# Kernel optimization log

Measured on AMD Instinct MI355X. Metric: run time of the kernel, lower is better.

Reference implementation:

```python
import jax, jax.numpy as jnp
import numpy as np

NPRE = 8        # diffusion iterations (production default 8000; math identical per step)
DEPS = 0.1
LAMBDA = 0.24
K_PM = 0.03     # exp(log(0.03)) buffer in the 'none' branch
ALPHA = 0.7
SIGMA_FREQ = 0.1


def _g_pm(x, K):
    # Perona-Malik conductance g(x) = 1 / (1 + |x^2| / K^2)
    return 1.0 / (1.0 + jnp.abs(x * x) / (K * K))


def _gaussian_blur3(x, sigma):
    # Replicates torch create_gaussian_kernel(3, sigma): linspace(-3//2, 3//2, 3) = [-2, -0.5, 1]
    xs = jnp.linspace(-2.0, 1.0, 3)
    g1 = jnp.exp(-(xs ** 2) / (2.0 * sigma * sigma))
    g1 = g1 / g1.sum()
    k2 = jnp.outer(g1, g1).astype(x.dtype)            # [3,3]
    C = x.shape[1]
    k = jnp.broadcast_to(k2, (C, 1, 3, 3))
    xp = jnp.pad(x, ((0, 0), (0, 0), (1, 1), (1, 1)), mode='reflect')
    return jax.lax.conv_general_dilated(
        xp, k, window_strides=(1, 1), padding='VALID',
        dimension_numbers=('NCHW', 'OIHW', 'NCHW'), feature_group_count=C)


def _edge_coeffs(I, K):
    # c(I): FFT high-pass edge response + finite differences -> Perona-Malik coefficients
    b, c_, h, w = I.shape
    F = jnp.fft.fft2(I, norm='ortho')
    y = jnp.linspace(-1.0, 1.0, h)[:, None]
    xg = jnp.linspace(-1.0, 1.0, w)[None, :]
    hf_mask = (jnp.sqrt(xg * xg + y * y) > 0.5).astype(I.dtype)   # [h,w]
    er = jnp.real(jnp.fft.ifft2(F * hf_mask, norm='ortho'))
    dv = jnp.abs(I[:, :, 1:, :] - I[:, :, :-1, :]) + er[:, :, 1:, :]
    dh = jnp.abs(I[:, :, :, 1:] - I[:, :, :, :-1]) + er[:, :, :, 1:]
    cv = _g_pm(jnp.mean(dv, axis=1, keepdims=True), K)   # [b,1,h-1,w]
    ch = _g_pm(jnp.mean(dh, axis=1, keepdims=True), K)   # [b,1,h,w-1]
    return cv, ch


def _diffuse_step(cv, ch, I, l=LAMBDA):
    # frequency-domain smoothing branch
    Ff = jnp.fft.fft2(I, norm='ortho')
    sr = _gaussian_blur3(jnp.real(Ff), SIGMA_FREQ)
    si = _gaussian_blur3(jnp.imag(Ff), SIGMA_FREQ)
    I_freq = jnp.real(jnp.fft.ifft2(jax.lax.complex(sr, si), norm='ortho'))
    dv = I[:, :, 1:, :] - I[:, :, :-1, :]
    dh = I[:, :, :, 1:] - I[:, :, :, :-1]
    I = ALPHA * I + (1.0 - ALPHA) * I_freq
    tv = l * cv * dv
    th = l * ch * dh
    I = I.at[:, :, 1:, :].add(-tv).at[:, :, :-1, :].add(tv)
    I = I.at[:, :, :, 1:].add(-th).at[:, :, :, :-1].add(th)
    return I


def _adjust_step(img, source, mask_inv, eps=1e-8):
    b, c_, h, w = img.shape
    sh, sw = source.shape[2], source.shape[3]
    fh, fw = h // sh, w // sw
    # AdaptiveAvgPool2d((sh,sw)) with integer factor == block mean
    img_ss = img.reshape(b, c_, sh, fh, sw, fw).mean(axis=(3, 5))
    ratio_ss = jnp.where(mask_inv, jnp.ones_like(img_ss), source / (img_ss + eps))
    # nearest upsample with integer factor == repeat
    ratio = jnp.repeat(jnp.repeat(ratio_ss, fh, axis=2), fw, axis=3)
    return img * ratio


def setup_inputs() -> dict:
    key = jax.random.key(0)
    k1, k2, k3, k4 = jax.random.split(key, 4)
    guide = jax.random.normal(k1, (4, 3, 1024, 1024), dtype=jnp.float32)
    source = jax.random.uniform(k2, (4, 1, 128, 128), dtype=jnp.float32)
    mask_lr = jax.random.uniform(k3, (4, 1, 128, 128), dtype=jnp.float32)
    y_bicubic = jax.random.uniform(k4, (4, 1, 1024, 1024), dtype=jnp.float32)
    return {"guide": guide, "source": source, "mask_lr": mask_lr, "y_bicubic": y_bicubic}


def reference(guide, source, mask_lr, y_bicubic):
    # depth shift when source.min() <= deps (uniform[0,1) source -> effectively always)
    shift = jnp.where(jnp.min(source) <= DEPS, DEPS, 0.0).astype(source.dtype)
    source = source + shift
    img = y_bicubic + shift
    mask_inv = mask_lr < 0.5

    # 'none' feature extractor: guide_feats = cat([guide, img], 1) -> [B,4,H,W]
    feats = jnp.concatenate([guide, img], axis=1)
    cv, ch = _edge_coeffs(feats, K_PM)

    def step(I, _):
        I = _diffuse_step(cv, ch, I)
        I = _adjust_step(I, source, mask_inv)
        return I, None

    img, _ = jax.lax.scan(step, img, None, length=NPRE)
    return img - shift
```

## Files before the change

### kernel.cpp

```cpp
#include <hip/hip_runtime.h>
#include <hip/hip_fp16.h>

namespace {

constexpr int H = 1024, W = 1024, NB = 4;
constexpr int SH = 128, SW = 128;
constexpr float LAM = 0.24f;
constexpr float KK = 0.03f * 0.03f;
constexpr float DEPS_V = 0.1f;
constexpr float FFT_SCALE = 1.0f / (1024.0f * 1024.0f);
constexpr int COL_LO = 256, NCOL = 512;

__device__ __forceinline__ float2 cadd(float2 a, float2 b) { return make_float2(a.x + b.x, a.y + b.y); }
__device__ __forceinline__ float2 csub(float2 a, float2 b) { return make_float2(a.x - b.x, a.y - b.y); }
__device__ __forceinline__ float2 cmul(float2 a, float2 b) {
  return make_float2(a.x * b.x - a.y * b.y, a.x * b.y + a.y * b.x);
}
__device__ __forceinline__ int phys2(int e) { return e + (e >> 4); }

__global__ void k_shift_part(const float* __restrict__ src, float* __restrict__ partial) {
  int t = threadIdx.x;
  int b0 = blockIdx.x * 1024;
  float m = fminf(fminf(src[b0 + t], src[b0 + t + 256]),
                  fminf(src[b0 + t + 512], src[b0 + t + 768]));
  for (int o = 32; o > 0; o >>= 1) m = fminf(m, __shfl_xor(m, o));
  __shared__ float sm[4];
  if ((t & 63) == 0) sm[t >> 6] = m;
  __syncthreads();
  if (t == 0) partial[blockIdx.x] = fminf(fminf(sm[0], sm[1]), fminf(sm[2], sm[3]));
}

__global__ void k_shift_fin(const float* __restrict__ partial, float* __restrict__ shiftp) {
  int t = threadIdx.x;
  float m = partial[t];
  for (int o = 32; o > 0; o >>= 1) m = fminf(m, __shfl_xor(m, o));
  if (t == 0) shiftp[0] = (m <= DEPS_V) ? DEPS_V : 0.0f;
}

template <int NS, bool INV>
__device__ __forceinline__ void r4_butterfly(float2 v[4], int j, float2 r[4]) {
  if (NS > 1) {
    int p = j & (NS - 1);
    float sn, cs;
    sincospif((INV ? 1.0f : -1.0f) * (float)p * (1.0f / (float)(2 * NS)), &sn, &cs);
    float2 w1 = make_float2(cs, sn);
    float2 w2 = cmul(w1, w1);
    float2 w3 = cmul(w2, w1);
    v[1] = cmul(v[1], w1);
    v[2] = cmul(v[2], w2);
    v[3] = cmul(v[3], w3);
  }
  float2 a0 = cadd(v[0], v[2]), a2 = csub(v[0], v[2]);
  float2 a1 = cadd(v[1], v[3]), a3 = csub(v[1], v[3]);
  a3 = INV ? make_float2(-a3.y, a3.x) : make_float2(a3.y, -a3.x);
  r[0] = cadd(a0, a1);
  r[2] = csub(a0, a1);
  r[1] = cadd(a2, a3);
  r[3] = csub(a2, a3);
}

template <int NS, bool INV>
__device__ __forceinline__ void r4_stage_lds(float2 v[4], float2* dst, int j) {
  float2 r[4];
  r4_butterfly<NS, INV>(v, j, r);
  int p = j & (NS - 1);
  int base = ((j - p) << 2) + p;
#pragma unroll
  for (int k = 0; k < 4; ++k) dst[phys2(base + k * NS)] = r[k];
}

__device__ __forceinline__ void lds_load4(const float2* src, float2 v[4], int j) {
#pragma unroll
  for (int k = 0; k < 4; ++k) v[k] = src[phys2(j + k * 256)];
}

template <bool INV>
__device__ void fft1024(float2 v[4], float2* b0, float2* b1, int j) {
  r4_stage_lds<1, INV>(v, b0, j);
  __syncthreads();
  lds_load4(b0, v, j);
  r4_stage_lds<4, INV>(v, b1, j);
  __syncthreads();
  lds_load4(b1, v, j);
  r4_stage_lds<16, INV>(v, b0, j);
  __syncthreads();
  lds_load4(b0, v, j);
  r4_stage_lds<64, INV>(v, b1, j);
  __syncthreads();
  lds_load4(b1, v, j);
  float2 r[4];
  r4_butterfly<256, INV>(v, j, r);
#pragma unroll
  for (int k = 0; k < 4; ++k) v[k] = r[k];
}

__global__ void k_rowfft_fwd(const float* __restrict__ guide, const float* __restrict__ ybic,
                             const float* __restrict__ shiftp, float2* __restrict__ A) {
  __shared__ float2 b0[1088], b1[1088];
  int b = blockIdx.y, y0 = blockIdx.x * 2, j = threadIdx.x;
  float sh = shiftp[0];
  const float* g0 = guide + ((size_t)(b * 3 + 0) * H + y0) * W;
  const float* g1 = guide + ((size_t)(b * 3 + 1) * H + y0) * W;
  const float* g2 = guide + ((size_t)(b * 3 + 2) * H + y0) * W;
  const float* yb = ybic + ((size_t)b * H + y0) * W;
  float2 v[4];
#pragma unroll
  for (int k = 0; k < 4; ++k) {
    int x = j + k * 256;
    float s0 = g0[x] + g1[x] + g2[x] + (yb[x] + sh);
    float s1 = g0[x + W] + g1[x + W] + g2[x + W] + (yb[x + W] + sh);
    v[k] = make_float2(s0, s1);
  }
  fft1024<false>(v, b0, b1, j);
#pragma unroll
  for (int k = 0; k < 4; ++k) b0[phys2(j + k * 256)] = v[k];
  __syncthreads();
  float2* o0 = A + ((size_t)b * H + y0) * W;
  float2* o1 = o0 + W;
#pragma unroll
  for (int k = 0; k < 4; ++k) {
    int m = j + k * 256;
    float2 Zm = v[k];
    float2 Zc = b0[phys2((1024 - m) & 1023)];
    o0[m] = make_float2(0.5f * (Zm.x + Zc.x), 0.5f * (Zm.y - Zc.y));
    o1[m] = make_float2(0.5f * (Zm.y + Zc.y), 0.5f * (Zc.x - Zm.x));
  }
}

__global__ void k_transpose_fwd(const float2* __restrict__ A, float2* __restrict__ Bc) {
  __shared__ float2 tile[32][33];
  int b = blockIdx.z;
  int c0 = blockIdx.x * 32, y0 = blockIdx.y * 32;
  const float2* ip = A + (size_t)b * H * W;
  float2* op = Bc + (size_t)b * NCOL * H;
#pragma unroll
  for (int k = 0; k < 4; ++k)
    tile[threadIdx.y + k * 8][threadIdx.x] =
        ip[(size_t)(y0 + threadIdx.y + k * 8) * W + (COL_LO + c0 + threadIdx.x)];
  __syncthreads();
#pragma unroll
  for (int k = 0; k < 4; ++k)
    op[(size_t)(c0 + threadIdx.y + k * 8) * H + (y0 + threadIdx.x)] =
        tile[threadIdx.x][threadIdx.y + k * 8];
}

__global__ void k_transpose_bwd(const float2* __restrict__ Bc, float2* __restrict__ A) {
  __shared__ float2 tile[32][33];
  int b = blockIdx.z;
  int c0 = blockIdx.x * 32, y0 = blockIdx.y * 32;
  const float2* ip = Bc + (size_t)b * NCOL * H;
  float2* op = A + (size_t)b * H * W;
#pragma unroll
  for (int k = 0; k < 4; ++k)
    tile[threadIdx.y + k * 8][threadIdx.x] =
        ip[(size_t)(c0 + threadIdx.y + k * 8) * H + (y0 + threadIdx.x)];
  __syncthreads();
#pragma unroll
  for (int k = 0; k < 4; ++k)
    op[(size_t)(y0 + threadIdx.y + k * 8) * W + (COL_LO + c0 + threadIdx.x)] =
        tile[threadIdx.x][threadIdx.y + k * 8];
}

__global__ void k_colfft_mask(float2* __restrict__ Bc) {
  __shared__ float2 b0[1088], b1[1088];
  int b = blockIdx.y, r = blockIdx.x, j = threadIdx.x;
  int k2 = COL_LO + r;
  double xj = -1.0 + 2.0 * (double)k2 / 1023.0;
  double xj2 = xj * xj;
  float2* row = Bc + ((size_t)b * NCOL + r) * H;
  float2 v[4];
#pragma unroll
  for (int k = 0; k < 4; ++k) v[k] = row[j + k * 256];
  fft1024<false>(v, b0, b1, j);
#pragma unroll
  for (int k = 0; k < 4; ++k) {
    int i = j + k * 256;
    double yv = -1.0 + 2.0 * (double)i / 1023.0;
    if (xj2 + yv * yv <= 0.25) v[k] = make_float2(0.0f, 0.0f);
  }
  fft1024<true>(v, b0, b1, j);
#pragma unroll
  for (int k = 0; k < 4; ++k) row[j + k * 256] = v[k];
}

__global__ void k_rowfft_inv(const float2* __restrict__ A, float* __restrict__ er) {
  __shared__ float2 b0[1088], b1[1088];
  int b = blockIdx.y, y = blockIdx.x, j = threadIdx.x;
  const float2* in = A + ((size_t)b * H + y) * W;
  float2 v[4];
#pragma unroll
  for (int k = 0; k < 4; ++k) v[k] = in[j + k * 256];
  v[0].x *= 1024.0f; v[0].y *= 1024.0f;
  v[3].x *= 1024.0f; v[3].y *= 1024.0f;
  fft1024<true>(v, b0, b1, j);
  float* out = er + ((size_t)b * H + y) * W;
#pragma unroll
  for (int k = 0; k < 4; ++k) out[j + k * 256] = v[k].x * FFT_SCALE;
}

__global__ void k_coeffs(const float* __restrict__ guide, const float* __restrict__ ybic,
                         const float* __restrict__ er, __half2* __restrict__ cvh) {
  int b = blockIdx.y, y = blockIdx.x, t = threadIdx.x;
  int x0 = t * 4;
  const float* g = guide + (size_t)b * 3 * H * W;
  const float* yb = ybic + (size_t)b * H * W;
  const float* e = er + (size_t)b * H * W;
  __half2* cp = cvh + (size_t)b * H * W;
  const size_t CH = (size_t)H * W;
  size_t row = (size_t)y * W + x0;
  float4 a0 = *(const float4*)(g + row);
  float4 a1 = *(const float4*)(g + CH + row);
  float4 a2 = *(const float4*)(g + 2 * CH + row);
  float4 a3 = *(const float4*)(yb + row);
  float4 e0 = *(const float4*)(e + row);
  float A0[5] = {a0.x, a0.y, a0.z, a0.w, 0.f};
  float A1[5] = {a1.x, a1.y, a1.z, a1.w, 0.f};
  float A2[5] = {a2.x, a2.y, a2.z, a2.w, 0.f};
  float A3[5] = {a3.x, a3.y, a3.z, a3.w, 0.f};
  float E0[5] = {e0.x, e0.y, e0.z, e0.w, 0.f};
  bool hasR = (x0 + 4 < W);
  if (hasR) {
    A0[4] = g[row + 4]; A1[4] = g[CH + row + 4]; A2[4] = g[2 * CH + row + 4];
    A3[4] = yb[row + 4]; E0[4] = e[row + 4];
  }
  float B0[4], B1[4], B2[4], B3[4], E1[4];
  bool hasD = (y < H - 1);
  if (hasD) {
    float4 q0 = *(const float4*)(g + row + W);
    float4 q1 = *(const float4*)(g + CH + row + W);
    float4 q2 = *(const float4*)(g + 2 * CH + row + W);
    float4 q3 = *(const float4*)(yb + row + W);
    float4 q4 = *(const float4*)(e + row + W);
    B0[0]=q0.x; B0[1]=q0.y; B0[2]=q0.z; B0[3]=q0.w;
    B1[0]=q1.x; B1[1]=q1.y; B1[2]=q1.z; B1[3]=q1.w;
    B2[0]=q2.x; B2[1]=q2.y; B2[2]=q2.z; B2[3]=q2.w;
    B3[0]=q3.x; B3[1]=q3.y; B3[2]=q3.z; B3[3]=q3.w;
    E1[0]=q4.x; E1[1]=q4.y; E1[2]=q4.z; E1[3]=q4.w;
  }
  __half2 outq[4];
#pragma unroll
  for (int i = 0; i < 4; ++i) {
    float cvv = 0.0f;
    if (hasD) {
      float s = fabsf(B0[i] - A0[i]) + fabsf(B1[i] - A1[i]) +
                fabsf(B2[i] - A2[i]) + fabsf(B3[i] - A3[i]);
      s = (s + E1[i]) * 0.25f;
      cvv = 1.0f / (1.0f + (s * s) / KK);
    }
    float chv = 0.0f;
    if (i < 3 || hasR) {
      float s = fabsf(A0[i + 1] - A0[i]) + fabsf(A1[i + 1] - A1[i]) +
                fabsf(A2[i + 1] - A2[i]) + fabsf(A3[i + 1] - A3[i]);
      s = (s + E0[i + 1]) * 0.25f;
      chv = 1.0f / (1.0f + (s * s) / KK);
    }
    outq[i] = __floats2half2_rn(cvv, chv);
  }
  *(float4*)(cp + row) = *(const float4*)outq;
}

template <bool FIRST, bool FINAL>
__global__ void k_diffuse_ratio(const float* __restrict__ in, const float* __restrict__ ratio_in,
                                const float* __restrict__ shiftp,
                                const __half2* __restrict__ cvh, const float* __restrict__ src,
                                const float* __restrict__ mask, float* __restrict__ out,
                                float* __restrict__ ratio_out) {
  int b = blockIdx.z, tx = threadIdx.x, ty = threadIdx.y;
  int x0 = blockIdx.x * 128 + tx * 4;
  int y = blockIdx.y * 8 + ty;
  float sh = shiftp[0];
  float addv = FIRST ? sh : 0.0f;
  size_t base = (size_t)b * H * W;
  const float* I = in + base;
  const __half2* cp = cvh + base;
  float rq = 1.f, rup = 1.f, rdn = 1.f, rlf = 1.f, rrt = 1.f;
  if (!FIRST) {
    const float* rb = ratio_in + (size_t)b * SH * SW;
    int bx3 = x0 >> 3, byq = y >> 3;
    rq = rb[byq * SW + bx3];
    rup = (y > 0) ? rb[((y - 1) >> 3) * SW + bx3] : 1.f;
    rdn = (y < H - 1) ? rb[((y + 1) >> 3) * SW + bx3] : 1.f;
    rlf = (x0 > 0) ? rb[byq * SW + ((x0 - 1) >> 3)] : 1.f;
    rrt = (x0 + 4 < W) ? rb[byq * SW + ((x0 + 4) >> 3)] : 1.f;
  }
  size_t row = (size_t)y * W + x0;
  bool hasU = (y > 0), hasD = (y < H - 1);
  float4 c4 = *(const float4*)(I + row);
  float C[4] = {(c4.x + addv) * rq, (c4.y + addv) * rq, (c4.z + addv) * rq, (c4.w + addv) * rq};
  float U[4] = {0, 0, 0, 0}, D[4] = {0, 0, 0, 0};
  if (hasU) {
    float4 u4 = *(const float4*)(I + row - W);
    U[0] = (u4.x + addv) * rup; U[1] = (u4.y + addv) * rup;
    U[2] = (u4.z + addv) * rup; U[3] = (u4.w + addv) * rup;
  }
  if (hasD) {
    float4 d4 = *(const float4*)(I + row + W);
    D[0] = (d4.x + addv) * rdn; D[1] = (d4.y + addv) * rdn;
    D[2] = (d4.z + addv) * rdn; D[3] = (d4.w + addv) * rdn;
  }
  float lf = (x0 > 0) ? (I[row - 1] + addv) * rlf : 0.f;
  float rt = (x0 + 4 < W) ? (I[row + 4] + addv) * rrt : 0.f;
  float4 ccraw = *(const float4*)(cp + row);
  const __half2* hq = (const __half2*)&ccraw;
  float cvq[4], chq[4];
#pragma unroll
  for (int i = 0; i < 4; ++i) {
    float2 tt = __half22float2(hq[i]);
    cvq[i] = tt.x; chq[i] = tt.y;
  }
  float cvu[4] = {0, 0, 0, 0};
  if (hasU) {
    float4 cu = *(const float4*)(cp + row - W);
    const __half2* hu = (const __half2*)&cu;
#pragma unroll
    for (int i = 0; i < 4; ++i) cvu[i] = __half2float(hu[i].x);
  }
  float chl = (x0 > 0) ? __half2float(cp[row - 1].y) : 0.f;
  float acc[4];
#pragma unroll
  for (int i = 0; i < 4; ++i) {
    float L = (i == 0) ? lf : C[i - 1];
    float R = (i == 3) ? rt : C[i + 1];
    float cL = (i == 0) ? chl : chq[i - 1];
    float a = C[i];
    if (hasD) a += LAM * cvq[i] * (D[i] - C[i]);
    if (hasU) a -= LAM * cvu[i] * (C[i] - U[i]);
    if (i < 3 || x0 + 4 < W) a += LAM * chq[i] * (R - C[i]);
    if (i > 0 || x0 > 0) a -= LAM * cL * (C[i] - L);
    acc[i] = a;
  }
  __shared__ float sd[8][32];
  __shared__ float rblk[16];
  sd[ty][tx] = acc[0] + acc[1] + acc[2] + acc[3];
  __syncthreads();
  if (ty == 0) {
    float colsum = 0.f;
#pragma unroll
    for (int r = 0; r < 8; ++r) colsum += sd[r][tx];
    float s = colsum + __shfl_down(colsum, 1);
    if ((tx & 1) == 0) {
      int pb = tx >> 1;
      size_t si = ((size_t)b * SH + blockIdx.y) * SW + (blockIdx.x * 16 + pb);
      float mean = s * (1.0f / 64.0f);
      float rv = (mask[si] < 0.5f) ? 1.0f : (src[si] + sh) / (mean + 1e-8f);
      if (FINAL) rblk[pb] = rv;
      else ratio_out[si] = rv;
    }
  }
  if (FINAL) {
    __syncthreads();
    float rv = rblk[tx >> 1];
    float4 o = make_float4(acc[0] * rv - sh, acc[1] * rv - sh, acc[2] * rv - sh, acc[3] * rv - sh);
    *(float4*)(out + base + row) = o;
  } else {
    *(float4*)(out + base + row) = make_float4(acc[0], acc[1], acc[2], acc[3]);
  }
}

}

extern "C" void kernel_launch(void* const* d_in, const int* in_sizes, int n_in, void* d_out,
                              int out_size, void* d_ws, size_t ws_size, hipStream_t stream) {
  (void)in_sizes; (void)n_in; (void)out_size; (void)ws_size;
  const float* guide = (const float*)d_in[0];
  const float* source = (const float*)d_in[1];
  const float* mask = (const float*)d_in[2];
  const float* ybic = (const float*)d_in[3];
  float* out = (float*)d_out;

  char* ws = (char*)d_ws;
  float2* A = (float2*)ws;
  float2* Bc = (float2*)(ws + (size_t)32 * 1024 * 1024);
  float* er = (float*)(ws + (size_t)32 * 1024 * 1024);
  __half2* cvh = (__half2*)(ws + (size_t)48 * 1024 * 1024);
  float* itmp = (float*)ws;
  float* shiftp = (float*)(ws + (size_t)64 * 1024 * 1024);
  float* partial = shiftp + 64;
  float* ratioA = (float*)(ws + (size_t)64 * 1024 * 1024 + 4096);
  float* ratioB = ratioA + (size_t)NB * SH * SW;

  k_shift_part<<<64, 256, 0, stream>>>(source, partial);
  k_shift_fin<<<1, 64, 0, stream>>>(partial, shiftp);

  k_rowfft_fwd<<<dim3(H / 2, NB), 256, 0, stream>>>(guide, ybic, shiftp, A);
  dim3 gT(NCOL / 32, H / 32, NB), bT(32, 8);
  k_transpose_fwd<<<gT, bT, 0, stream>>>(A, Bc);
  k_colfft_mask<<<dim3(NCOL, NB), 256, 0, stream>>>(Bc);
  k_transpose_bwd<<<gT, bT, 0, stream>>>(Bc, A);
  k_rowfft_inv<<<dim3(H, NB), 256, 0, stream>>>(A, er);

  k_coeffs<<<dim3(H, NB), 256, 0, stream>>>(guide, ybic, er, cvh);

  dim3 gD(W / 128, H / 8, NB), bD(32, 8);
  k_diffuse_ratio<true, false><<<gD, bD, 0, stream>>>(ybic, nullptr, shiftp, cvh, source, mask,
                                                      itmp, ratioA);
  k_diffuse_ratio<false, false><<<gD, bD, 0, stream>>>(itmp, ratioA, shiftp, cvh, source, mask,
                                                       out, ratioB);
  k_diffuse_ratio<false, false><<<gD, bD, 0, stream>>>(out, ratioB, shiftp, cvh, source, mask,
                                                       itmp, ratioA);
  k_diffuse_ratio<false, false><<<gD, bD, 0, stream>>>(itmp, ratioA, shiftp, cvh, source, mask,
                                                       out, ratioB);
  k_diffuse_ratio<false, false><<<gD, bD, 0, stream>>>(out, ratioB, shiftp, cvh, source, mask,
                                                       itmp, ratioA);
  k_diffuse_ratio<false, false><<<gD, bD, 0, stream>>>(itmp, ratioA, shiftp, cvh, source, mask,
                                                       out, ratioB);
  k_diffuse_ratio<false, false><<<gD, bD, 0, stream>>>(out, ratioB, shiftp, cvh, source, mask,
                                                       itmp, ratioA);
  k_diffuse_ratio<false, true><<<gD, bD, 0, stream>>>(itmp, ratioA, shiftp, cvh, source, mask,
                                                      out, ratioB);
}
```

Baseline: 296.1 us.

## Fuse pairs of diffusion steps per launch using halo recomputation in LDS

Each launch now computes two diffusion+ratio-adjust steps. It first computes the first step over a 48x144 haloed tile into shared memory, then derives the intermediate block ratios from it and applies the second step on the inner 32x128 tile. This halves the number of diffusion launches and the global round-trips of the full image between steps. In exchange it recomputes halo cells redundantly, does scalar global loads for the first step, and uses a large shared-memory footprint that may limit occupancy.

```diff
diff --git a/kernel.cpp b/kernel.cpp
--- a/kernel.cpp
+++ b/kernel.cpp
@@ -260,100 +260,167 @@
 }
 
 template <bool FIRST, bool FINAL>
-__global__ void k_diffuse_ratio(const float* __restrict__ in, const float* __restrict__ ratio_in,
-                                const float* __restrict__ shiftp,
-                                const __half2* __restrict__ cvh, const float* __restrict__ src,
-                                const float* __restrict__ mask, float* __restrict__ out,
-                                float* __restrict__ ratio_out) {
-  int b = blockIdx.z, tx = threadIdx.x, ty = threadIdx.y;
-  int x0 = blockIdx.x * 128 + tx * 4;
-  int y = blockIdx.y * 8 + ty;
-  float sh = shiftp[0];
-  float addv = FIRST ? sh : 0.0f;
-  size_t base = (size_t)b * H * W;
+__global__ __launch_bounds__(256, 4) void k_diffuse2(
+    const float* __restrict__ in, const float* __restrict__ ratio_in,
+    const float* __restrict__ shiftp, const __half2* __restrict__ cvh,
+    const float* __restrict__ src, const float* __restrict__ mask,
+    float* __restrict__ out, float* __restrict__ ratio_out) {
+  __shared__ float s_acc[48][145];
+  __shared__ float s_rin[8][20];
+  __shared__ float s_ratio[6][18];
+  __shared__ float s_sum[8][32];
+  __shared__ float s_rblk[4][16];
+  const int b = blockIdx.z, tx = threadIdx.x, ty = threadIdx.y;
+  const int tid = ty * 32 + tx;
+  const int C0 = blockIdx.x * 128, R0 = blockIdx.y * 32;
+  const float sh = shiftp[0];
+  const float add = FIRST ? sh : 0.0f;
+  const size_t base = (size_t)b * H * W;
   const float* I = in + base;
   const __half2* cp = cvh + base;
-  float rq = 1.f, rup = 1.f, rdn = 1.f, rlf = 1.f, rrt = 1.f;
+
   if (!FIRST) {
-    const float* rb = ratio_in + (size_t)b * SH * SW;
-    int bx3 = x0 >> 3, byq = y >> 3;
-    rq = rb[byq * SW + bx3];
-    rup = (y > 0) ? rb[((y - 1) >> 3) * SW + bx3] : 1.f;
-    rdn = (y < H - 1) ? rb[((y + 1) >> 3) * SW + bx3] : 1.f;
-    rlf = (x0 > 0) ? rb[byq * SW + ((x0 - 1) >> 3)] : 1.f;
-    rrt = (x0 + 4 < W) ? rb[byq * SW + ((x0 + 4) >> 3)] : 1.f;
-  }
-  size_t row = (size_t)y * W + x0;
-  bool hasU = (y > 0), hasD = (y < H - 1);
-  float4 c4 = *(const float4*)(I + row);
-  float C[4] = {(c4.x + addv) * rq, (c4.y + addv) * rq, (c4.z + addv) * rq, (c4.w + addv) * rq};
-  float U[4] = {0, 0, 0, 0}, D[4] = {0, 0, 0, 0};
-  if (hasU) {
-    float4 u4 = *(const float4*)(I + row - W);
-    U[0] = (u4.x + addv) * rup; U[1] = (u4.y + addv) * rup;
-    U[2] = (u4.z + addv) * rup; U[3] = (u4.w + addv) * rup;
-  }
-  if (hasD) {
-    float4 d4 = *(const float4*)(I + row + W);
-    D[0] = (d4.x + addv) * rdn; D[1] = (d4.y + addv) * rdn;
-    D[2] = (d4.z + addv) * rdn; D[3] = (d4.w + addv) * rdn;
-  }
-  float lf = (x0 > 0) ? (I[row - 1] + addv) * rlf : 0.f;
-  float rt = (x0 + 4 < W) ? (I[row + 4] + addv) * rrt : 0.f;
-  float4 ccraw = *(const float4*)(cp + row);
-  const __half2* hq = (const __half2*)&ccraw;
-  float cvq[4], chq[4];
-#pragma unroll
-  for (int i = 0; i < 4; ++i) {
-    float2 tt = __half22float2(hq[i]);
-    cvq[i] = tt.x; chq[i] = tt.y;
-  }
-  float cvu[4] = {0, 0, 0, 0};
-  if (hasU) {
-    float4 cu = *(const float4*)(cp + row - W);
-    const __half2* hu = (const __half2*)&cu;
-#pragma unroll
-    for (int i = 0; i < 4; ++i) cvu[i] = __half2float(hu[i].x);
-  }
-  float chl = (x0 > 0) ? __half2float(cp[row - 1].y) : 0.f;
-  float acc[4];
-#pragma unroll
-  for (int i = 0; i < 4; ++i) {
-    float L = (i == 0) ? lf : C[i - 1];
-    float R = (i == 3) ? rt : C[i + 1];
-    float cL = (i == 0) ? chl : chq[i - 1];
-    float a = C[i];
-    if (hasD) a += LAM * cvq[i] * (D[i] - C[i]);
-    if (hasU) a -= LAM * cvu[i] * (C[i] - U[i]);
-    if (i < 3 || x0 + 4 < W) a += LAM * chq[i] * (R - C[i]);
-    if (i > 0 || x0 > 0) a -= LAM * cL * (C[i] - L);
-    acc[i] = a;
-  }
-  __shared__ float sd[8][32];
-  __shared__ float rblk[16];
-  sd[ty][tx] = acc[0] + acc[1] + acc[2] + acc[3];
-  __syncthreads();
-  if (ty == 0) {
-    float colsum = 0.f;
-#pragma unroll
-    for (int r = 0; r < 8; ++r) colsum += sd[r][tx];
-    float s = colsum + __shfl_down(colsum, 1);
-    if ((tx & 1) == 0) {
-      int pb = tx >> 1;
-      size_t si = ((size_t)b * SH + blockIdx.y) * SW + (blockIdx.x * 16 + pb);
-      float mean = s * (1.0f / 64.0f);
-      float rv = (mask[si] < 0.5f) ? 1.0f : (src[si] + sh) / (mean + 1e-8f);
-      if (FINAL) rblk[pb] = rv;
-      else ratio_out[si] = rv;
-    }
-  }
+    if (tid < 160) {
+      int lr = tid / 20, lc = tid - lr * 20;
+      int gr = (R0 >> 3) - 2 + lr, gc = (C0 >> 3) - 2 + lc;
+      float v = 1.0f;
+      if (gr >= 0 && gr < SH && gc >= 0 && gc < SW)
+        v = ratio_in[((size_t)b * SH + gr) * SW + gc];
+      s_rin[lr][lc] = v;
+    }
+    __syncthreads();
+  }
+
+  for (int rr = ty; rr < 48; rr += 8) {
+    int y = R0 - 8 + rr;
+    if ((unsigned)y >= (unsigned)H) continue;
+    for (int cc = tx; cc < 144; cc += 32) {
+      int x = C0 - 8 + cc;
+      if ((unsigned)x >= (unsigned)W) continue;
+      float rq = 1.f, ru = 1.f, rd = 1.f, rl = 1.f, rr2 = 1.f;
+      if (!FIRST) {
+        int pr = (rr >> 3) + 1, pc = (cc >> 3) + 1;
+        rq = s_rin[pr][pc];
+        ru = s_rin[((rr - 1) >> 3) + 1][pc];
+        rd = s_rin[((rr + 1) >> 3) + 1][pc];
+        rl = s_rin[pr][((cc - 1) >> 3) + 1];
+        rr2 = s_rin[pr][((cc + 1) >> 3) + 1];
+      }
+      size_t ri = (size_t)y * W + x;
+      float C = (I[ri] + add) * rq;
+      float2 co = __half22float2(cp[ri]);
+      float a = C;
+      if (y < H - 1) { float D = (I[ri + W] + add) * rd; a += LAM * co.x * (D - C); }
+      if (y > 0) { float U = (I[ri - W] + add) * ru; float cu = __half2float(cp[ri - W].x); a -= LAM * cu * (C - U); }
+      if (x < W - 1) { float Rv = (I[ri + 1] + add) * rr2; a += LAM * co.y * (Rv - C); }
+      if (x > 0) { float L = (I[ri - 1] + add) * rl; float cl = __half2float(cp[ri - 1].y); a -= LAM * cl * (C - L); }
+      s_acc[rr][cc] = a;
+    }
+  }
+  __syncthreads();
+
+  if (tid < 108) {
+    int pr = tid / 18, pc = tid - pr * 18;
+    int gr = (R0 >> 3) - 1 + pr, gc = (C0 >> 3) - 1 + pc;
+    float rv = 1.0f;
+    if (gr >= 0 && gr < SH && gc >= 0 && gc < SW) {
+      float s = 0.f;
+#pragma unroll
+      for (int i = 0; i < 8; ++i)
+#pragma unroll
+        for (int jj = 0; jj < 8; ++jj) s += s_acc[pr * 8 + i][pc * 8 + jj];
+      size_t si = ((size_t)b * SH + gr) * SW + gc;
+      rv = (mask[si] < 0.5f) ? 1.0f : (src[si] + sh) / (s * (1.0f / 64.0f) + 1e-8f);
+    }
+    s_ratio[pr][pc] = rv;
+  }
+  __syncthreads();
+
+  const int x0 = C0 + tx * 4;
+  const int lc = tx * 4 + 8;
+  float acc2[4][4];
+#pragma unroll
+  for (int r = 0; r < 4; ++r) {
+    int yy = R0 + ty * 4 + r;
+    int lr = ty * 4 + r + 8;
+    bool hasU = yy > 0, hasD = yy < H - 1;
+    float rq = s_ratio[lr >> 3][lc >> 3];
+    float ru = s_ratio[(lr - 1) >> 3][lc >> 3];
+    float rd = s_ratio[(lr + 1) >> 3][lc >> 3];
+    float rl = s_ratio[lr >> 3][(lc - 1) >> 3];
+    float rr2 = s_ratio[lr >> 3][(lc + 4) >> 3];
+    size_t ri = (size_t)yy * W + x0;
+    float4 c4 = *(const float4*)(cp + ri);
+    const __half2* hq = (const __half2*)&c4;
+    float cvq[4], chq[4];
+#pragma unroll
+    for (int i = 0; i < 4; ++i) { float2 t = __half22float2(hq[i]); cvq[i] = t.x; chq[i] = t.y; }
+    float cvu[4] = {0, 0, 0, 0};
+    if (hasU) {
+      float4 u4 = *(const float4*)(cp + ri - W);
+      const __half2* hu = (const __half2*)&u4;
+#pragma unroll
+      for (int i = 0; i < 4; ++i) cvu[i] = __half2float(hu[i].x);
+    }
+    float chl = (x0 > 0) ? __half2float(cp[ri - 1].y) : 0.f;
+    float Cv[4], Uv[4], Dv[4];
+#pragma unroll
+    for (int i = 0; i < 4; ++i) Cv[i] = s_acc[lr][lc + i] * rq;
+#pragma unroll
+    for (int i = 0; i < 4; ++i) Uv[i] = hasU ? s_acc[lr - 1][lc + i] * ru : 0.f;
+#pragma unroll
+    for (int i = 0; i < 4; ++i) Dv[i] = hasD ? s_acc[lr + 1][lc + i] * rd : 0.f;
+    float lf = (x0 > 0) ? s_acc[lr][lc - 1] * rl : 0.f;
+    float rt = (x0 + 4 < W) ? s_acc[lr][lc + 4] * rr2 : 0.f;
+#pragma unroll
+    for (int i = 0; i < 4; ++i) {
+      float L = (i == 0) ? lf : Cv[i - 1];
+      float Rv = (i == 3) ? rt : Cv[i + 1];
+      float cL = (i == 0) ? chl : chq[i - 1];
+      float a = Cv[i];
+      if (hasD) a += LAM * cvq[i] * (Dv[i] - Cv[i]);
+      if (hasU) a -= LAM * cvu[i] * (Cv[i] - Uv[i]);
+      if (i < 3 || x0 + 4 < W) a += LAM * chq[i] * (Rv - Cv[i]);
+      if (i > 0 || x0 > 0) a -= LAM * cL * (Cv[i] - L);
+      acc2[r][i] = a;
+    }
+  }
+
+  float part = 0.f;
+#pragma unroll
+  for (int r = 0; r < 4; ++r)
+#pragma unroll
+    for (int i = 0; i < 4; ++i) part += acc2[r][i];
+  s_sum[ty][tx] = part;
+  __syncthreads();
+  if (tid < 64) {
+    int pby = tid >> 4, pbx = tid & 15;
+    float s = s_sum[2 * pby][2 * pbx] + s_sum[2 * pby][2 * pbx + 1] +
+              s_sum[2 * pby + 1][2 * pbx] + s_sum[2 * pby + 1][2 * pbx + 1];
+    int gr = (R0 >> 3) + pby, gc = (C0 >> 3) + pbx;
+    size_t si = ((size_t)b * SH + gr) * SW + gc;
+    float rv = (mask[si] < 0.5f) ? 1.0f : (src[si] + sh) / (s * (1.0f / 64.0f) + 1e-8f);
+    if (FINAL) s_rblk[pby][pbx] = rv;
+    else ratio_out[si] = rv;
+  }
+  float* op = out + base;
   if (FINAL) {
     __syncthreads();
-    float rv = rblk[tx >> 1];
-    float4 o = make_float4(acc[0] * rv - sh, acc[1] * rv - sh, acc[2] * rv - sh, acc[3] * rv - sh);
-    *(float4*)(out + base + row) = o;
+    float rv = s_rblk[ty >> 1][tx >> 1];
+#pragma unroll
+    for (int r = 0; r < 4; ++r) {
+      int yy = R0 + ty * 4 + r;
+      *(float4*)(op + (size_t)yy * W + x0) =
+          make_float4(acc2[r][0] * rv - sh, acc2[r][1] * rv - sh,
+                      acc2[r][2] * rv - sh, acc2[r][3] * rv - sh);
+    }
   } else {
-    *(float4*)(out + base + row) = make_float4(acc[0], acc[1], acc[2], acc[3]);
+#pragma unroll
+    for (int r = 0; r < 4; ++r) {
+      int yy = R0 + ty * 4 + r;
+      *(float4*)(op + (size_t)yy * W + x0) =
+          make_float4(acc2[r][0], acc2[r][1], acc2[r][2], acc2[r][3]);
+    }
   }
 }
 
@@ -391,21 +458,13 @@
 
   k_coeffs<<<dim3(H, NB), 256, 0, stream>>>(guide, ybic, er, cvh);
 
-  dim3 gD(W / 128, H / 8, NB), bD(32, 8);
-  k_diffuse_ratio<true, false><<<gD, bD, 0, stream>>>(ybic, nullptr, shiftp, cvh, source, mask,
-                                                      itmp, ratioA);
-  k_diffuse_ratio<false, false><<<gD, bD, 0, stream>>>(itmp, ratioA, shiftp, cvh, source, mask,
-                                                       out, ratioB);
-  k_diffuse_ratio<false, false><<<gD, bD, 0, stream>>>(out, ratioB, shiftp, cvh, source, mask,
-                                                       itmp, ratioA);
-  k_diffuse_ratio<false, false><<<gD, bD, 0, stream>>>(itmp, ratioA, shiftp, cvh, source, mask,
-                                                       out, ratioB);
-  k_diffuse_ratio<false, false><<<gD, bD, 0, stream>>>(out, ratioB, shiftp, cvh, source, mask,
-                                                       itmp, ratioA);
-  k_diffuse_ratio<false, false><<<gD, bD, 0, stream>>>(itmp, ratioA, shiftp, cvh, source, mask,
-                                                       out, ratioB);
-  k_diffuse_ratio<false, false><<<gD, bD, 0, stream>>>(out, ratioB, shiftp, cvh, source, mask,
-                                                       itmp, ratioA);
-  k_diffuse_ratio<false, true><<<gD, bD, 0, stream>>>(itmp, ratioA, shiftp, cvh, source, mask,
-                                                      out, ratioB);
-}
+  dim3 gD2(W / 128, H / 32, NB), bD2(32, 8);
+  k_diffuse2<true, false><<<gD2, bD2, 0, stream>>>(ybic, nullptr, shiftp, cvh, source, mask,
+                                                   itmp, ratioA);
+  k_diffuse2<false, false><<<gD2, bD2, 0, stream>>>(itmp, ratioA, shiftp, cvh, source, mask,
+                                                    out, ratioB);
+  k_diffuse2<false, false><<<gD2, bD2, 0, stream>>>(out, ratioB, shiftp, cvh, source, mask,
+                                                    itmp, ratioA);
+  k_diffuse2<false, true><<<gD2, bD2, 0, stream>>>(itmp, ratioA, shiftp, cvh, source, mask,
+                                                   out, nullptr);
+}
```

New measurement: 388.6 us. 31.2% more time.

## Fuse backward transpose, inverse row FFT, and coefficient computation into one kernel

Applied to the files above, without the earlier changes.

Removes the backward transpose and the separate inverse-row-FFT and coefficient kernels, replacing them with one kernel that handles 4 output rows per block. Each block reads the column-FFT results directly from the transposed buffer into shared memory, runs the inverse row FFTs (5 rows, one row of overlap), and keeps the edge response in a double-buffered shared array instead of writing it to global memory. This drops a full transpose pass and the global er round trip. In exchange, each block recomputes one extra FFT row, does its FFTs serially, and has a larger shared-memory footprint.

```diff
diff --git a/kernel.cpp b/kernel.cpp
--- a/kernel.cpp
+++ b/kernel.cpp
@@ -144,23 +144,6 @@
         tile[threadIdx.x][threadIdx.y + k * 8];
 }
 
-__global__ void k_transpose_bwd(const float2* __restrict__ Bc, float2* __restrict__ A) {
-  __shared__ float2 tile[32][33];
-  int b = blockIdx.z;
-  int c0 = blockIdx.x * 32, y0 = blockIdx.y * 32;
-  const float2* ip = Bc + (size_t)b * NCOL * H;
-  float2* op = A + (size_t)b * H * W;
-#pragma unroll
-  for (int k = 0; k < 4; ++k)
-    tile[threadIdx.y + k * 8][threadIdx.x] =
-        ip[(size_t)(c0 + threadIdx.y + k * 8) * H + (y0 + threadIdx.x)];
-  __syncthreads();
-#pragma unroll
-  for (int k = 0; k < 4; ++k)
-    op[(size_t)(y0 + threadIdx.y + k * 8) * W + (COL_LO + c0 + threadIdx.x)] =
-        tile[threadIdx.x][threadIdx.y + k * 8];
-}
-
 __global__ void k_colfft_mask(float2* __restrict__ Bc) {
   __shared__ float2 b0[1088], b1[1088];
   int b = blockIdx.y, r = blockIdx.x, j = threadIdx.x;
@@ -183,80 +166,107 @@
   for (int k = 0; k < 4; ++k) row[j + k * 256] = v[k];
 }
 
-__global__ void k_rowfft_inv(const float2* __restrict__ A, float* __restrict__ er) {
+__global__ __launch_bounds__(256, 3) void k_invcoeffs(
+    const float2* __restrict__ A, const float2* __restrict__ Bc,
+    const float* __restrict__ guide, const float* __restrict__ ybic,
+    __half2* __restrict__ cvh) {
   __shared__ float2 b0[1088], b1[1088];
-  int b = blockIdx.y, y = blockIdx.x, j = threadIdx.x;
-  const float2* in = A + ((size_t)b * H + y) * W;
-  float2 v[4];
-#pragma unroll
-  for (int k = 0; k < 4; ++k) v[k] = in[j + k * 256];
-  v[0].x *= 1024.0f; v[0].y *= 1024.0f;
-  v[3].x *= 1024.0f; v[3].y *= 1024.0f;
-  fft1024<true>(v, b0, b1, j);
-  float* out = er + ((size_t)b * H + y) * W;
-#pragma unroll
-  for (int k = 0; k < 4; ++k) out[j + k * 256] = v[k].x * FFT_SCALE;
-}
-
-__global__ void k_coeffs(const float* __restrict__ guide, const float* __restrict__ ybic,
-                         const float* __restrict__ er, __half2* __restrict__ cvh) {
-  int b = blockIdx.y, y = blockIdx.x, t = threadIdx.x;
-  int x0 = t * 4;
+  __shared__ float2 stage[5][NCOL];
+  __shared__ float erbuf[2][1028];
+  const int b = blockIdx.y, j = threadIdx.x;
+  const int y0 = blockIdx.x * 4;
+  const float2* Ab = A + (size_t)b * H * W;
   const float* g = guide + (size_t)b * 3 * H * W;
   const float* yb = ybic + (size_t)b * H * W;
-  const float* e = er + (size_t)b * H * W;
-  __half2* cp = cvh + (size_t)b * H * W;
+  __half2* cpo = cvh + (size_t)b * H * W;
   const size_t CH = (size_t)H * W;
-  size_t row = (size_t)y * W + x0;
-  float4 a0 = *(const float4*)(g + row);
-  float4 a1 = *(const float4*)(g + CH + row);
-  float4 a2 = *(const float4*)(g + 2 * CH + row);
-  float4 a3 = *(const float4*)(yb + row);
-  float4 e0 = *(const float4*)(e + row);
-  float A0[5] = {a0.x, a0.y, a0.z, a0.w, 0.f};
-  float A1[5] = {a1.x, a1.y, a1.z, a1.w, 0.f};
-  float A2[5] = {a2.x, a2.y, a2.z, a2.w, 0.f};
-  float A3[5] = {a3.x, a3.y, a3.z, a3.w, 0.f};
-  float E0[5] = {e0.x, e0.y, e0.z, e0.w, 0.f};
-  bool hasR = (x0 + 4 < W);
-  if (hasR) {
-    A0[4] = g[row + 4]; A1[4] = g[CH + row + 4]; A2[4] = g[2 * CH + row + 4];
-    A3[4] = yb[row + 4]; E0[4] = e[row + 4];
-  }
-  float B0[4], B1[4], B2[4], B3[4], E1[4];
-  bool hasD = (y < H - 1);
-  if (hasD) {
-    float4 q0 = *(const float4*)(g + row + W);
-    float4 q1 = *(const float4*)(g + CH + row + W);
-    float4 q2 = *(const float4*)(g + 2 * CH + row + W);
-    float4 q3 = *(const float4*)(yb + row + W);
-    float4 q4 = *(const float4*)(e + row + W);
-    B0[0]=q0.x; B0[1]=q0.y; B0[2]=q0.z; B0[3]=q0.w;
-    B1[0]=q1.x; B1[1]=q1.y; B1[2]=q1.z; B1[3]=q1.w;
-    B2[0]=q2.x; B2[1]=q2.y; B2[2]=q2.z; B2[3]=q2.w;
-    B3[0]=q3.x; B3[1]=q3.y; B3[2]=q3.z; B3[3]=q3.w;
-    E1[0]=q4.x; E1[1]=q4.y; E1[2]=q4.z; E1[3]=q4.w;
-  }
-  __half2 outq[4];
-#pragma unroll
-  for (int i = 0; i < 4; ++i) {
-    float cvv = 0.0f;
-    if (hasD) {
-      float s = fabsf(B0[i] - A0[i]) + fabsf(B1[i] - A1[i]) +
-                fabsf(B2[i] - A2[i]) + fabsf(B3[i] - A3[i]);
-      s = (s + E1[i]) * 0.25f;
-      cvv = 1.0f / (1.0f + (s * s) / KK);
+
+#pragma unroll
+  for (int cc = 0; cc < 2; ++cc) {
+    int c = j + cc * 256;
+    const float2* bp = Bc + ((size_t)b * NCOL + c) * H + y0;
+    float4 p01 = *(const float4*)bp;
+    float4 p23 = *(const float4*)(bp + 2);
+    float2 p4 = (y0 + 4 < H) ? bp[4] : make_float2(0.f, 0.f);
+    stage[0][c] = make_float2(p01.x, p01.y);
+    stage[1][c] = make_float2(p01.z, p01.w);
+    stage[2][c] = make_float2(p23.x, p23.y);
+    stage[3][c] = make_float2(p23.z, p23.w);
+    stage[4][c] = p4;
+  }
+  __syncthreads();
+
+  const int x0 = j * 4;
+  for (int r = 0; r < 5; ++r) {
+    int yf = y0 + r;
+    if (yf < H) {
+      const float2* arow = Ab + (size_t)yf * W;
+      float2 v[4];
+      float2 a0 = arow[j], a3 = arow[j + 768];
+      v[0] = make_float2(a0.x * 1024.0f, a0.y * 1024.0f);
+      v[3] = make_float2(a3.x * 1024.0f, a3.y * 1024.0f);
+      v[1] = stage[r][j];
+      v[2] = stage[r][j + 256];
+      fft1024<true>(v, b0, b1, j);
+#pragma unroll
+      for (int k = 0; k < 4; ++k) erbuf[r & 1][j + k * 256] = v[k].x * FFT_SCALE;
     }
-    float chv = 0.0f;
-    if (i < 3 || hasR) {
-      float s = fabsf(A0[i + 1] - A0[i]) + fabsf(A1[i + 1] - A1[i]) +
-                fabsf(A2[i + 1] - A2[i]) + fabsf(A3[i + 1] - A3[i]);
-      s = (s + E0[i + 1]) * 0.25f;
-      chv = 1.0f / (1.0f + (s * s) / KK);
+    __syncthreads();
+    if (r >= 1) {
+      int y = y0 + r - 1;
+      size_t row = (size_t)y * W + x0;
+      float4 a0 = *(const float4*)(g + row);
+      float4 a1 = *(const float4*)(g + CH + row);
+      float4 a2 = *(const float4*)(g + 2 * CH + row);
+      float4 a3 = *(const float4*)(yb + row);
+      float4 e0 = *(const float4*)&erbuf[(r - 1) & 1][x0];
+      float A0[5] = {a0.x, a0.y, a0.z, a0.w, 0.f};
+      float A1[5] = {a1.x, a1.y, a1.z, a1.w, 0.f};
+      float A2[5] = {a2.x, a2.y, a2.z, a2.w, 0.f};
+      float A3[5] = {a3.x, a3.y, a3.z, a3.w, 0.f};
+      float E0[5] = {e0.x, e0.y, e0.z, e0.w, 0.f};
+      bool hasR = (x0 + 4 < W);
+      if (hasR) {
+        A0[4] = g[row + 4]; A1[4] = g[CH + row + 4]; A2[4] = g[2 * CH + row + 4];
+        A3[4] = yb[row + 4]; E0[4] = erbuf[(r - 1) & 1][x0 + 4];
+      }
+      float B0[4], B1[4], B2[4], B3[4], E1[4];
+      bool hasD = (y < H - 1);
+      if (hasD) {
+        float4 q0 = *(const float4*)(g + row + W);
+        float4 q1 = *(const float4*)(g + CH + row + W);
+        float4 q2 = *(const float4*)(g + 2 * CH + row + W);
+        float4 q3 = *(const float4*)(yb + row + W);
+        float4 q4 = *(const float4*)&erbuf[r & 1][x0];
+        B0[0]=q0.x; B0[1]=q0.y; B0[2]=q0.z; B0[3]=q0.w;
+        B1[0]=q1.x; B1[1]=q1.y; B1[2]=q1.z; B1[3]=q1.w;
+        B2[0]=q2.x; B2[1]=q2.y; B2[2]=q2.z; B2[3]=q2.w;
+        B3[0]=q3.x; B3[1]=q3.y; B3[2]=q3.z; B3[3]=q3.w;
+        E1[0]=q4.x; E1[1]=q4.y; E1[2]=q4.z; E1[3]=q4.w;
+      }
+      __half2 outq[4];
+#pragma unroll
+      for (int i = 0; i < 4; ++i) {
+        float cvv = 0.0f;
+        if (hasD) {
+          float s = fabsf(B0[i] - A0[i]) + fabsf(B1[i] - A1[i]) +
+                    fabsf(B2[i] - A2[i]) + fabsf(B3[i] - A3[i]);
+          s = (s + E1[i]) * 0.25f;
+          cvv = 1.0f / (1.0f + (s * s) / KK);
+        }
+        float chv = 0.0f;
+        if (i < 3 || hasR) {
+          float s = fabsf(A0[i + 1] - A0[i]) + fabsf(A1[i + 1] - A1[i]) +
+                    fabsf(A2[i + 1] - A2[i]) + fabsf(A3[i + 1] - A3[i]);
+          s = (s + E0[i + 1]) * 0.25f;
+          chv = 1.0f / (1.0f + (s * s) / KK);
+        }
+        outq[i] = __floats2half2_rn(cvv, chv);
+      }
+      *(float4*)(cpo + row) = *(const float4*)outq;
     }
-    outq[i] = __floats2half2_rn(cvv, chv);
-  }
-  *(float4*)(cp + row) = *(const float4*)outq;
+    __syncthreads();
+  }
 }
 
 template <bool FIRST, bool FINAL>
@@ -371,7 +381,6 @@
   char* ws = (char*)d_ws;
   float2* A = (float2*)ws;
   float2* Bc = (float2*)(ws + (size_t)32 * 1024 * 1024);
-  float* er = (float*)(ws + (size_t)32 * 1024 * 1024);
   __half2* cvh = (__half2*)(ws + (size_t)48 * 1024 * 1024);
   float* itmp = (float*)ws;
   float* shiftp = (float*)(ws + (size_t)64 * 1024 * 1024);
@@ -386,10 +395,7 @@
   dim3 gT(NCOL / 32, H / 32, NB), bT(32, 8);
   k_transpose_fwd<<<gT, bT, 0, stream>>>(A, Bc);
   k_colfft_mask<<<dim3(NCOL, NB), 256, 0, stream>>>(Bc);
-  k_transpose_bwd<<<gT, bT, 0, stream>>>(Bc, A);
-  k_rowfft_inv<<<dim3(H, NB), 256, 0, stream>>>(A, er);
-
-  k_coeffs<<<dim3(H, NB), 256, 0, stream>>>(guide, ybic, er, cvh);
+  k_invcoeffs<<<dim3(H / 4, NB), 256, 0, stream>>>(A, Bc, guide, ybic, cvh);
 
   dim3 gD(W / 128, H / 8, NB), bD(32, 8);
   k_diffuse_ratio<true, false><<<gD, bD, 0, stream>>>(ybic, nullptr, shiftp, cvh, source, mask,
```

Result: faster. 290.2 us (-2.0%).
